# Optimization experiments

Measured on AMD Instinct MI355X. Metric: run time of the kernel, lower is better.

Reference implementation:

```python
import jax, jax.numpy as jnp
import numpy as np

FEAT = 2048
NUM_CLASSES = 751
EPS = 1e-5


def setup_inputs() -> dict:
    key = jax.random.key(0)
    k1, k2, k3 = jax.random.split(key, 3)
    probe_x = jax.random.normal(k1, (64, FEAT), dtype=jnp.float32)
    gallery_x = jax.random.normal(k2, (256, FEAT), dtype=jnp.float32)
    # BatchNorm1d affine params (PyTorch init: gamma=1, beta=0)
    bn_gamma = jnp.ones((FEAT,), dtype=jnp.float32)
    bn_beta = jnp.zeros((FEAT,), dtype=jnp.float32)
    # classifier: weight ~ N(0, 0.001), bias = 0
    W = jax.random.normal(k3, (NUM_CLASSES, FEAT), dtype=jnp.float32) * 0.001
    b = jnp.zeros((NUM_CLASSES,), dtype=jnp.float32)
    return {"probe_x": probe_x, "gallery_x": gallery_x,
            "bn_gamma": bn_gamma, "bn_beta": bn_beta, "W": W, "b": b}


def reference(probe_x, gallery_x, bn_gamma, bn_beta, W, b):
    n_probe, feat = probe_x.shape
    n_gallery = gallery_x.shape[0]
    # broadcast squared difference: [Np, Ng, F]
    diff = jnp.square(probe_x[:, None, :] - gallery_x[None, :, :])
    d = diff.reshape(n_probe * n_gallery, feat)
    # BatchNorm1d in training mode: biased batch statistics over the batch dim
    mean = jnp.mean(d, axis=0)
    var = jnp.mean(jnp.square(d - mean), axis=0)
    bn = (d - mean) * (bn_gamma / jnp.sqrt(var + EPS)) + bn_beta
    # Linear classifier
    cls = jnp.einsum('nf,cf->nc', bn, W) + b
    return cls.reshape(n_probe, n_gallery, -1)
```

## Files before the change

kernel.cpp:

```cpp
#include <hip/hip_runtime.h>
#include <hip/hip_bf16.h>
#include <hip/hip_fp16.h>

#define FEAT 2048
#define NCLS 751
#define NPAD 768
#define NPRB 64
#define NGAL 256
#define WSCALE 256.0f

typedef _Float16 f16x8 __attribute__((ext_vector_type(8)));
typedef float f32x4 __attribute__((ext_vector_type(4)));

__device__ __forceinline__ unsigned short f2h_u(float x) {
  union { _Float16 h; unsigned short u; } v;
  v.h = (_Float16)x;
  return v.u;
}

__global__ void stats_kernel(const float* __restrict__ P, const float* __restrict__ G,
                             const float* __restrict__ gamma, const float* __restrict__ beta,
                             float* __restrict__ st) {
  int fx = threadIdx.x & 31, ry = threadIdx.x >> 5;
  int f = blockIdx.x * 32 + fx;
  float a1 = 0, a2 = 0, a3 = 0, a4 = 0;
  for (int r = ry; r < NPRB; r += 8) {
    float x = P[r * FEAT + f], x2 = x * x;
    a1 += x; a2 += x2; a3 += x2 * x; a4 += x2 * x2;
  }
  float b1 = 0, b2 = 0, b3 = 0, b4 = 0;
  for (int r = ry; r < NGAL; r += 8) {
    float x = G[r * FEAT + f], x2 = x * x;
    b1 += x; b2 += x2; b3 += x2 * x; b4 += x2 * x2;
  }
  __shared__ float red[8][8][32];
  float vals[8] = {a1, a2, a3, a4, b1, b2, b3, b4};
#pragma unroll
  for (int m = 0; m < 8; ++m) red[m][ry][fx] = vals[m];
  __syncthreads();
  if (ry == 0) {
    float mm[8];
#pragma unroll
    for (int m = 0; m < 8; ++m) {
      float sum = 0.f;
#pragma unroll
      for (int r = 0; r < 8; ++r) sum += red[m][r][fx];
      mm[m] = sum;
    }
    float M1p = mm[0] * (1.f / NPRB), M2p = mm[1] * (1.f / NPRB);
    float M3p = mm[2] * (1.f / NPRB), M4p = mm[3] * (1.f / NPRB);
    float M1g = mm[4] * (1.f / NGAL), M2g = mm[5] * (1.f / NGAL);
    float M3g = mm[6] * (1.f / NGAL), M4g = mm[7] * (1.f / NGAL);
    float mean = M2p - 2.f * M1p * M1g + M2g;
    float Ed2 = M4p - 4.f * M3p * M1g + 6.f * M2p * M2g - 4.f * M1p * M3g + M4g;
    float var = Ed2 - mean * mean;
    float sv = gamma[f] / sqrtf(var + 1e-5f);
    st[f] = sv;
    st[FEAT + f] = beta[f] - mean * sv;
  }
}

__global__ void prepb_kernel(const float* __restrict__ W, const float* __restrict__ st,
                             unsigned short* __restrict__ Wp) {
  int idx = (blockIdx.x * 256 + threadIdx.x) * 4;
  int c = idx >> 11, f = idx & (FEAT - 1);
  float4 w = make_float4(0.f, 0.f, 0.f, 0.f);
  if (c < NCLS) w = *(const float4*)(W + (size_t)c * FEAT + f);
  float4 sv = *(const float4*)(st + f);
  unsigned int u0 = (unsigned int)f2h_u(w.x * sv.x * WSCALE) |
                    ((unsigned int)f2h_u(w.y * sv.y * WSCALE) << 16);
  unsigned int u1 = (unsigned int)f2h_u(w.z * sv.z * WSCALE) |
                    ((unsigned int)f2h_u(w.w * sv.w * WSCALE) << 16);
  uint2 u; u.x = u0; u.y = u1;
  *(uint2*)(Wp + idx) = u;
}

__global__ void prepbias_kernel(const float* __restrict__ W, const float* __restrict__ b,
                                const float* __restrict__ st, float* __restrict__ bp) {
  int c = blockIdx.x;
  const float* t = st + FEAT;
  float acc = 0.f;
  for (int f = threadIdx.x; f < FEAT; f += 256) acc += t[f] * W[(size_t)c * FEAT + f];
#pragma unroll
  for (int off = 32; off > 0; off >>= 1) acc += __shfl_down(acc, off, 64);
  __shared__ float r[4];
  int wave = threadIdx.x >> 6, lane = threadIdx.x & 63;
  if (lane == 0) r[wave] = acc;
  __syncthreads();
  if (threadIdx.x == 0) bp[c] = b[c] + r[0] + r[1] + r[2] + r[3];
}

#define AS_STRIDE 56

__global__ __launch_bounds__(256, 3)
void gemm_kernel(const float* __restrict__ P, const float* __restrict__ G,
                 const unsigned short* __restrict__ Wp, const float* __restrict__ bp,
                 float* __restrict__ out) {
  __shared__ float Prow[FEAT];
  __shared__ unsigned short As[128 * AS_STRIDE];
  __shared__ unsigned short Bs[128 * 32];

  const int tid = threadIdx.x;
  const int lane = tid & 63, wave = tid >> 6;
  const int mtile = blockIdx.x, ntile = blockIdx.y;
  const int p = mtile >> 1;
  const int g0 = (mtile & 1) * 128;

  const float4* psrc = (const float4*)(P + (size_t)p * FEAT);
  ((float4*)Prow)[tid] = psrc[tid];
  ((float4*)Prow)[tid + 256] = psrc[tid + 256];

  f32x4 acc[4][4];
#pragma unroll
  for (int mi = 0; mi < 4; ++mi)
#pragma unroll
    for (int ni = 0; ni < 4; ++ni) acc[mi][ni] = (f32x4){0.f, 0.f, 0.f, 0.f};

  const int wm = (wave & 1) * 64, wn = (wave >> 1) * 64;

  const int arow = tid >> 3, ac4 = tid & 7;
  const float* gbase = G + (size_t)(g0 + arow) * FEAT + ac4 * 4;
  unsigned short* awr = As + arow * AS_STRIDE + ac4 * 4;

  const int brow = tid >> 2, bchk = tid & 3;
  const unsigned short* bgbase = Wp + (size_t)(ntile * 128 + brow) * FEAT + bchk * 8;
  char* blds0 = (char*)Bs + wave * 1024;

  for (int k0 = 0; k0 < FEAT; k0 += 32) {
    __syncthreads();
    __builtin_amdgcn_global_load_lds(
        (const __attribute__((address_space(1))) void*)(bgbase + k0),
        (__attribute__((address_space(3))) void*)(blds0), 16, 0, 0);
    __builtin_amdgcn_global_load_lds(
        (const __attribute__((address_space(1))) void*)(bgbase + 64 * FEAT + k0),
        (__attribute__((address_space(3))) void*)(blds0 + 4096), 16, 0, 0);
    float4 p4 = *(const float4*)(Prow + k0 + ac4 * 4);
#pragma unroll
    for (int j = 0; j < 4; ++j) {
      float4 g4 = *(const float4*)(gbase + (size_t)j * 32 * FEAT + k0);
      float dx = p4.x - g4.x, dy = p4.y - g4.y;
      float dz = p4.z - g4.z, dw = p4.w - g4.w;
      uint2 u;
      u.x = (unsigned int)f2h_u(dx * dx) | ((unsigned int)f2h_u(dy * dy) << 16);
      u.y = (unsigned int)f2h_u(dz * dz) | ((unsigned int)f2h_u(dw * dw) << 16);
      *(uint2*)(awr + j * 32 * AS_STRIDE) = u;
    }
    __syncthreads();
    f16x8 af[4], bf[4];
#pragma unroll
    for (int mi = 0; mi < 4; ++mi)
      af[mi] = *(const f16x8*)(As + (wm + mi * 16 + (lane & 15)) * AS_STRIDE + (lane >> 4) * 8);
#pragma unroll
    for (int ni = 0; ni < 4; ++ni)
      bf[ni] = *(const f16x8*)(Bs + (wn + ni * 16 + (lane & 15)) * 32 + (lane >> 4) * 8);
#pragma unroll
    for (int mi = 0; mi < 4; ++mi)
#pragma unroll
      for (int ni = 0; ni < 4; ++ni)
        acc[mi][ni] = __builtin_amdgcn_mfma_f32_16x16x32_f16(af[mi], bf[ni], acc[mi][ni], 0, 0, 0);
  }

  const int col0 = ntile * 128 + wn + (lane & 15);
  const int row0 = mtile * 128 + wm + ((lane >> 4) << 2);
#pragma unroll
  for (int ni = 0; ni < 4; ++ni) {
    int col = col0 + ni * 16;
    if (col >= NCLS) continue;
    float bv = bp[col];
#pragma unroll
    for (int mi = 0; mi < 4; ++mi) {
      int row = row0 + mi * 16;
#pragma unroll
      for (int r = 0; r < 4; ++r)
        out[(size_t)(row + r) * NCLS + col] = acc[mi][ni][r] * (1.0f / WSCALE) + bv;
    }
  }
}

extern "C" void kernel_launch(void* const* d_in, const int* in_sizes, int n_in,
                              void* d_out, int out_size, void* d_ws, size_t ws_size,
                              hipStream_t stream) {
  const float* P = (const float*)d_in[0];
  const float* G = (const float*)d_in[1];
  const float* gamma = (const float*)d_in[2];
  const float* beta = (const float*)d_in[3];
  const float* W = (const float*)d_in[4];
  const float* b = (const float*)d_in[5];
  float* out = (float*)d_out;

  float* st = (float*)d_ws;
  float* bp = st + 2 * FEAT;
  unsigned short* Wp = (unsigned short*)(bp + NPAD);

  hipLaunchKernelGGL(stats_kernel, dim3(64), dim3(256), 0, stream, P, G, gamma, beta, st);
  hipLaunchKernelGGL(prepb_kernel, dim3(NPAD * FEAT / 1024), dim3(256), 0, stream, W, st, Wp);
  hipLaunchKernelGGL(prepbias_kernel, dim3(NCLS), dim3(256), 0, stream, W, b, st, bp);
  hipLaunchKernelGGL(gemm_kernel, dim3(128, 6), dim3(256), 0, stream, P, G, Wp, bp, out);
}
```

Baseline: 184.4 us.

## Materialize fp16 squared-difference matrix then run plain GEMM

Adds a kernel that writes the full probe-gallery squared-difference matrix in fp16 to workspace. A simpler GEMM then streams both operands via direct global-to-LDS loads. This removes the per-tile on-the-fly conversion that was repeated for every class tile. In exchange it adds a large extra write and read of a 64 MB intermediate. The old fused kernel is kept as a fallback when the workspace is too small.

```diff
diff --git a/kernel.cpp b/kernel.cpp
--- a/kernel.cpp
+++ b/kernel.cpp
@@ -90,12 +90,103 @@
   if (threadIdx.x == 0) bp[c] = b[c] + r[0] + r[1] + r[2] + r[3];
 }
 
+__global__ void agen_kernel(const float* __restrict__ P, const float* __restrict__ G,
+                            unsigned short* __restrict__ A) {
+  int n = blockIdx.x;
+  int p = n >> 8, g = n & 255;
+  int f = threadIdx.x * 8;
+  const float4* p4 = (const float4*)(P + (size_t)p * FEAT + f);
+  const float4* g4 = (const float4*)(G + (size_t)g * FEAT + f);
+  float4 pa = p4[0], pb = p4[1];
+  float4 ga = g4[0], gb = g4[1];
+  float d0 = pa.x - ga.x, d1 = pa.y - ga.y, d2 = pa.z - ga.z, d3 = pa.w - ga.w;
+  float d4 = pb.x - gb.x, d5 = pb.y - gb.y, d6 = pb.z - gb.z, d7 = pb.w - gb.w;
+  uint4 u;
+  u.x = (unsigned int)f2h_u(d0 * d0) | ((unsigned int)f2h_u(d1 * d1) << 16);
+  u.y = (unsigned int)f2h_u(d2 * d2) | ((unsigned int)f2h_u(d3 * d3) << 16);
+  u.z = (unsigned int)f2h_u(d4 * d4) | ((unsigned int)f2h_u(d5 * d5) << 16);
+  u.w = (unsigned int)f2h_u(d6 * d6) | ((unsigned int)f2h_u(d7 * d7) << 16);
+  *(uint4*)(A + (size_t)n * FEAT + f) = u;
+}
+
+__global__ __launch_bounds__(256, 3)
+void gemm_mat_kernel(const unsigned short* __restrict__ A,
+                     const unsigned short* __restrict__ Wp,
+                     const float* __restrict__ bp, float* __restrict__ out) {
+  __shared__ unsigned short As[128 * 32];
+  __shared__ unsigned short Bs[128 * 32];
+
+  const int tid = threadIdx.x;
+  const int lane = tid & 63, wave = tid >> 6;
+  const int mtile = blockIdx.x, ntile = blockIdx.y;
+
+  const int srow = tid >> 2, schk = tid & 3;
+  const unsigned short* ag = A + (size_t)(mtile * 128 + srow) * FEAT + schk * 8;
+  const unsigned short* bg = Wp + (size_t)(ntile * 128 + srow) * FEAT + schk * 8;
+  char* alds = (char*)As + wave * 1024;
+  char* blds = (char*)Bs + wave * 1024;
+
+  f32x4 acc[4][4];
+#pragma unroll
+  for (int mi = 0; mi < 4; ++mi)
+#pragma unroll
+    for (int ni = 0; ni < 4; ++ni) acc[mi][ni] = (f32x4){0.f, 0.f, 0.f, 0.f};
+
+  const int wm = (wave & 1) * 64, wn = (wave >> 1) * 64;
+
+  for (int k0 = 0; k0 < FEAT; k0 += 32) {
+    __syncthreads();
+    __builtin_amdgcn_global_load_lds(
+        (const __attribute__((address_space(1))) void*)(ag + k0),
+        (__attribute__((address_space(3))) void*)(alds), 16, 0, 0);
+    __builtin_amdgcn_global_load_lds(
+        (const __attribute__((address_space(1))) void*)(ag + (size_t)64 * FEAT + k0),
+        (__attribute__((address_space(3))) void*)(alds + 4096), 16, 0, 0);
+    __builtin_amdgcn_global_load_lds(
+        (const __attribute__((address_space(1))) void*)(bg + k0),
+        (__attribute__((address_space(3))) void*)(blds), 16, 0, 0);
+    __builtin_amdgcn_global_load_lds(
+        (const __attribute__((address_space(1))) void*)(bg + (size_t)64 * FEAT + k0),
+        (__attribute__((address_space(3))) void*)(blds + 4096), 16, 0, 0);
+    __syncthreads();
+
+    f16x8 af[4], bf[4];
+#pragma unroll
+    for (int mi = 0; mi < 4; ++mi)
+      af[mi] = *(const f16x8*)(As + (wm + mi * 16 + (lane & 15)) * 32 + (lane >> 4) * 8);
+#pragma unroll
+    for (int ni = 0; ni < 4; ++ni)
+      bf[ni] = *(const f16x8*)(Bs + (wn + ni * 16 + (lane & 15)) * 32 + (lane >> 4) * 8);
+#pragma unroll
+    for (int mi = 0; mi < 4; ++mi)
+#pragma unroll
+      for (int ni = 0; ni < 4; ++ni)
+        acc[mi][ni] = __builtin_amdgcn_mfma_f32_16x16x32_f16(af[mi], bf[ni], acc[mi][ni], 0, 0, 0);
+  }
+
+  const int col0 = ntile * 128 + wn + (lane & 15);
+  const int row0 = mtile * 128 + wm + ((lane >> 4) << 2);
+#pragma unroll
+  for (int ni = 0; ni < 4; ++ni) {
+    int col = col0 + ni * 16;
+    if (col >= NCLS) continue;
+    float bv = bp[col];
+#pragma unroll
+    for (int mi = 0; mi < 4; ++mi) {
+      int row = row0 + mi * 16;
+#pragma unroll
+      for (int r = 0; r < 4; ++r)
+        out[(size_t)(row + r) * NCLS + col] = acc[mi][ni][r] * (1.0f / WSCALE) + bv;
+    }
+  }
+}
+
 #define AS_STRIDE 56
 
 __global__ __launch_bounds__(256, 3)
-void gemm_kernel(const float* __restrict__ P, const float* __restrict__ G,
-                 const unsigned short* __restrict__ Wp, const float* __restrict__ bp,
-                 float* __restrict__ out) {
+void gemm_fly_kernel(const float* __restrict__ P, const float* __restrict__ G,
+                     const unsigned short* __restrict__ Wp, const float* __restrict__ bp,
+                     float* __restrict__ out) {
   __shared__ float Prow[FEAT];
   __shared__ unsigned short As[128 * AS_STRIDE];
   __shared__ unsigned short Bs[128 * 32];
@@ -117,11 +208,9 @@
     for (int ni = 0; ni < 4; ++ni) acc[mi][ni] = (f32x4){0.f, 0.f, 0.f, 0.f};
 
   const int wm = (wave & 1) * 64, wn = (wave >> 1) * 64;
-
   const int arow = tid >> 3, ac4 = tid & 7;
   const float* gbase = G + (size_t)(g0 + arow) * FEAT + ac4 * 4;
   unsigned short* awr = As + arow * AS_STRIDE + ac4 * 4;
-
   const int brow = tid >> 2, bchk = tid & 3;
   const unsigned short* bgbase = Wp + (size_t)(ntile * 128 + brow) * FEAT + bchk * 8;
   char* blds0 = (char*)Bs + wave * 1024;
@@ -191,9 +280,19 @@
   float* st = (float*)d_ws;
   float* bp = st + 2 * FEAT;
   unsigned short* Wp = (unsigned short*)(bp + NPAD);
+  unsigned short* A = Wp + (size_t)NPAD * FEAT;
+
+  size_t need = (size_t)(2 * FEAT + NPAD) * 4 + (size_t)NPAD * FEAT * 2 +
+                (size_t)NPRB * NGAL * FEAT * 2;
 
   hipLaunchKernelGGL(stats_kernel, dim3(64), dim3(256), 0, stream, P, G, gamma, beta, st);
   hipLaunchKernelGGL(prepb_kernel, dim3(NPAD * FEAT / 1024), dim3(256), 0, stream, W, st, Wp);
   hipLaunchKernelGGL(prepbias_kernel, dim3(NCLS), dim3(256), 0, stream, W, b, st, bp);
-  hipLaunchKernelGGL(gemm_kernel, dim3(128, 6), dim3(256), 0, stream, P, G, Wp, bp, out);
-}
+
+  if (ws_size >= need) {
+    hipLaunchKernelGGL(agen_kernel, dim3(NPRB * NGAL), dim3(256), 0, stream, P, G, A);
+    hipLaunchKernelGGL(gemm_mat_kernel, dim3(128, 6), dim3(256), 0, stream, A, Wp, bp, out);
+  } else {
+    hipLaunchKernelGGL(gemm_fly_kernel, dim3(128, 6), dim3(256), 0, stream, P, G, Wp, bp, out);
+  }
+}
```

Result: faster. 179.6 us (-2.6%).

## Materialize fp16 squared-difference matrix and stream both GEMM operands via LDS DMA

Applied to the files above, without the earlier changes.

Adds a separate kernel that writes the full 16384x2048 fp16 squared-difference matrix to workspace, so the GEMM loads both A and B with global_load_lds and an XOR-swizzled LDS layout instead of computing A inline from P and G. The K step grows from 32 to 64, which halves the barrier count. The W prep and bias kernels are merged into one kernel. The cost is writing and re-reading about 64 MB of A, read once per N tile, in exchange for removing per-tile VALU conversion and global float loads from the GEMM's critical path.

```diff
diff --git a/kernel.cpp b/kernel.cpp
--- a/kernel.cpp
+++ b/kernel.cpp
@@ -60,55 +60,73 @@
   }
 }
 
-__global__ void prepb_kernel(const float* __restrict__ W, const float* __restrict__ st,
-                             unsigned short* __restrict__ Wp) {
-  int idx = (blockIdx.x * 256 + threadIdx.x) * 4;
-  int c = idx >> 11, f = idx & (FEAT - 1);
-  float4 w = make_float4(0.f, 0.f, 0.f, 0.f);
-  if (c < NCLS) w = *(const float4*)(W + (size_t)c * FEAT + f);
-  float4 sv = *(const float4*)(st + f);
-  unsigned int u0 = (unsigned int)f2h_u(w.x * sv.x * WSCALE) |
-                    ((unsigned int)f2h_u(w.y * sv.y * WSCALE) << 16);
-  unsigned int u1 = (unsigned int)f2h_u(w.z * sv.z * WSCALE) |
-                    ((unsigned int)f2h_u(w.w * sv.w * WSCALE) << 16);
-  uint2 u; u.x = u0; u.y = u1;
-  *(uint2*)(Wp + idx) = u;
-}
-
-__global__ void prepbias_kernel(const float* __restrict__ W, const float* __restrict__ b,
-                                const float* __restrict__ st, float* __restrict__ bp) {
+__global__ void prepw_kernel(const float* __restrict__ W, const float* __restrict__ b,
+                             const float* __restrict__ st,
+                             unsigned short* __restrict__ Wp, float* __restrict__ bp) {
   int c = blockIdx.x;
-  const float* t = st + FEAT;
-  float acc = 0.f;
-  for (int f = threadIdx.x; f < FEAT; f += 256) acc += t[f] * W[(size_t)c * FEAT + f];
+  int f = threadIdx.x * 8;
+  float4 w0 = make_float4(0.f, 0.f, 0.f, 0.f), w1 = w0;
+  if (c < NCLS) {
+    const float4* wsrc = (const float4*)(W + (size_t)c * FEAT + f);
+    w0 = wsrc[0]; w1 = wsrc[1];
+  }
+  const float4* s4 = (const float4*)(st + f);
+  float4 s0 = s4[0], s1 = s4[1];
+  const float4* t4 = (const float4*)(st + FEAT + f);
+  float4 t0 = t4[0], t1 = t4[1];
+  uint4 u;
+  u.x = (unsigned int)f2h_u(w0.x * s0.x * WSCALE) | ((unsigned int)f2h_u(w0.y * s0.y * WSCALE) << 16);
+  u.y = (unsigned int)f2h_u(w0.z * s0.z * WSCALE) | ((unsigned int)f2h_u(w0.w * s0.w * WSCALE) << 16);
+  u.z = (unsigned int)f2h_u(w1.x * s1.x * WSCALE) | ((unsigned int)f2h_u(w1.y * s1.y * WSCALE) << 16);
+  u.w = (unsigned int)f2h_u(w1.z * s1.z * WSCALE) | ((unsigned int)f2h_u(w1.w * s1.w * WSCALE) << 16);
+  *(uint4*)(Wp + (size_t)c * FEAT + f) = u;
+  float acc = t0.x * w0.x + t0.y * w0.y + t0.z * w0.z + t0.w * w0.w +
+              t1.x * w1.x + t1.y * w1.y + t1.z * w1.z + t1.w * w1.w;
 #pragma unroll
   for (int off = 32; off > 0; off >>= 1) acc += __shfl_down(acc, off, 64);
   __shared__ float r[4];
   int wave = threadIdx.x >> 6, lane = threadIdx.x & 63;
   if (lane == 0) r[wave] = acc;
   __syncthreads();
-  if (threadIdx.x == 0) bp[c] = b[c] + r[0] + r[1] + r[2] + r[3];
-}
-
-#define AS_STRIDE 56
+  if (threadIdx.x == 0) bp[c] = (c < NCLS ? b[c] : 0.f) + r[0] + r[1] + r[2] + r[3];
+}
+
+__global__ void agen_kernel(const float* __restrict__ P, const float* __restrict__ G,
+                            unsigned short* __restrict__ A) {
+  int n = blockIdx.x;
+  int p = n >> 8, g = n & 255;
+  int f = threadIdx.x * 8;
+  const float4* p4 = (const float4*)(P + (size_t)p * FEAT + f);
+  const float4* g4 = (const float4*)(G + (size_t)g * FEAT + f);
+  float4 pa = p4[0], pb = p4[1];
+  float4 ga = g4[0], gb = g4[1];
+  float d0 = pa.x - ga.x, d1 = pa.y - ga.y, d2 = pa.z - ga.z, d3 = pa.w - ga.w;
+  float d4 = pb.x - gb.x, d5 = pb.y - gb.y, d6 = pb.z - gb.z, d7 = pb.w - gb.w;
+  uint4 u;
+  u.x = (unsigned int)f2h_u(d0 * d0) | ((unsigned int)f2h_u(d1 * d1) << 16);
+  u.y = (unsigned int)f2h_u(d2 * d2) | ((unsigned int)f2h_u(d3 * d3) << 16);
+  u.z = (unsigned int)f2h_u(d4 * d4) | ((unsigned int)f2h_u(d5 * d5) << 16);
+  u.w = (unsigned int)f2h_u(d6 * d6) | ((unsigned int)f2h_u(d7 * d7) << 16);
+  *(uint4*)(A + (size_t)n * FEAT + f) = u;
+}
 
 __global__ __launch_bounds__(256, 3)
-void gemm_kernel(const float* __restrict__ P, const float* __restrict__ G,
-                 const unsigned short* __restrict__ Wp, const float* __restrict__ bp,
-                 float* __restrict__ out) {
-  __shared__ float Prow[FEAT];
-  __shared__ unsigned short As[128 * AS_STRIDE];
-  __shared__ unsigned short Bs[128 * 32];
+void gemm_mat_kernel(const unsigned short* __restrict__ A,
+                     const unsigned short* __restrict__ Wp,
+                     const float* __restrict__ bp, float* __restrict__ out) {
+  __shared__ unsigned short As[128 * 64];
+  __shared__ unsigned short Bs[128 * 64];
 
   const int tid = threadIdx.x;
   const int lane = tid & 63, wave = tid >> 6;
   const int mtile = blockIdx.x, ntile = blockIdx.y;
-  const int p = mtile >> 1;
-  const int g0 = (mtile & 1) * 128;
-
-  const float4* psrc = (const float4*)(P + (size_t)p * FEAT);
-  ((float4*)Prow)[tid] = psrc[tid];
-  ((float4*)Prow)[tid + 256] = psrc[tid + 256];
+
+  const int srow = tid >> 3;
+  const int sch = (tid & 7) ^ (srow & 7);
+  const unsigned short* ag = A + (size_t)(mtile * 128 + srow) * FEAT + sch * 8;
+  const unsigned short* bg = Wp + (size_t)(ntile * 128 + srow) * FEAT + sch * 8;
+  char* alds = (char*)As + wave * 1024;
+  char* blds = (char*)Bs + wave * 1024;
 
   f32x4 acc[4][4];
 #pragma unroll
@@ -117,47 +135,37 @@
     for (int ni = 0; ni < 4; ++ni) acc[mi][ni] = (f32x4){0.f, 0.f, 0.f, 0.f};
 
   const int wm = (wave & 1) * 64, wn = (wave >> 1) * 64;
-
-  const int arow = tid >> 3, ac4 = tid & 7;
-  const float* gbase = G + (size_t)(g0 + arow) * FEAT + ac4 * 4;
-  unsigned short* awr = As + arow * AS_STRIDE + ac4 * 4;
-
-  const int brow = tid >> 2, bchk = tid & 3;
-  const unsigned short* bgbase = Wp + (size_t)(ntile * 128 + brow) * FEAT + bchk * 8;
-  char* blds0 = (char*)Bs + wave * 1024;
-
-  for (int k0 = 0; k0 < FEAT; k0 += 32) {
+  const int frow = lane & 15, fsw = lane & 7, fk = lane >> 4;
+
+  for (int k0 = 0; k0 < FEAT; k0 += 64) {
     __syncthreads();
-    __builtin_amdgcn_global_load_lds(
-        (const __attribute__((address_space(1))) void*)(bgbase + k0),
-        (__attribute__((address_space(3))) void*)(blds0), 16, 0, 0);
-    __builtin_amdgcn_global_load_lds(
-        (const __attribute__((address_space(1))) void*)(bgbase + 64 * FEAT + k0),
-        (__attribute__((address_space(3))) void*)(blds0 + 4096), 16, 0, 0);
-    float4 p4 = *(const float4*)(Prow + k0 + ac4 * 4);
 #pragma unroll
     for (int j = 0; j < 4; ++j) {
-      float4 g4 = *(const float4*)(gbase + (size_t)j * 32 * FEAT + k0);
-      float dx = p4.x - g4.x, dy = p4.y - g4.y;
-      float dz = p4.z - g4.z, dw = p4.w - g4.w;
-      uint2 u;
-      u.x = (unsigned int)f2h_u(dx * dx) | ((unsigned int)f2h_u(dy * dy) << 16);
-      u.y = (unsigned int)f2h_u(dz * dz) | ((unsigned int)f2h_u(dw * dw) << 16);
-      *(uint2*)(awr + j * 32 * AS_STRIDE) = u;
+      __builtin_amdgcn_global_load_lds(
+          (const __attribute__((address_space(1))) void*)(ag + k0 + (size_t)j * 32 * FEAT),
+          (__attribute__((address_space(3))) void*)(alds + j * 4096), 16, 0, 0);
+      __builtin_amdgcn_global_load_lds(
+          (const __attribute__((address_space(1))) void*)(bg + k0 + (size_t)j * 32 * FEAT),
+          (__attribute__((address_space(3))) void*)(blds + j * 4096), 16, 0, 0);
     }
     __syncthreads();
-    f16x8 af[4], bf[4];
-#pragma unroll
-    for (int mi = 0; mi < 4; ++mi)
-      af[mi] = *(const f16x8*)(As + (wm + mi * 16 + (lane & 15)) * AS_STRIDE + (lane >> 4) * 8);
-#pragma unroll
-    for (int ni = 0; ni < 4; ++ni)
-      bf[ni] = *(const f16x8*)(Bs + (wn + ni * 16 + (lane & 15)) * 32 + (lane >> 4) * 8);
-#pragma unroll
-    for (int mi = 0; mi < 4; ++mi)
+
+#pragma unroll
+    for (int kk = 0; kk < 2; ++kk) {
+      const int slot = (kk * 4 + fk) ^ fsw;
+      f16x8 af[4], bf[4];
+#pragma unroll
+      for (int mi = 0; mi < 4; ++mi)
+        af[mi] = *(const f16x8*)(As + (wm + mi * 16 + frow) * 64 + slot * 8);
 #pragma unroll
       for (int ni = 0; ni < 4; ++ni)
-        acc[mi][ni] = __builtin_amdgcn_mfma_f32_16x16x32_f16(af[mi], bf[ni], acc[mi][ni], 0, 0, 0);
+        bf[ni] = *(const f16x8*)(Bs + (wn + ni * 16 + frow) * 64 + slot * 8);
+#pragma unroll
+      for (int mi = 0; mi < 4; ++mi)
+#pragma unroll
+        for (int ni = 0; ni < 4; ++ni)
+          acc[mi][ni] = __builtin_amdgcn_mfma_f32_16x16x32_f16(af[mi], bf[ni], acc[mi][ni], 0, 0, 0);
+    }
   }
 
   const int col0 = ntile * 128 + wn + (lane & 15);
@@ -191,9 +199,10 @@
   float* st = (float*)d_ws;
   float* bp = st + 2 * FEAT;
   unsigned short* Wp = (unsigned short*)(bp + NPAD);
-
+  unsigned short* A = Wp + (size_t)NPAD * FEAT;
+
+  hipLaunchKernelGGL(agen_kernel, dim3(NPRB * NGAL), dim3(256), 0, stream, P, G, A);
   hipLaunchKernelGGL(stats_kernel, dim3(64), dim3(256), 0, stream, P, G, gamma, beta, st);
-  hipLaunchKernelGGL(prepb_kernel, dim3(NPAD * FEAT / 1024), dim3(256), 0, stream, W, st, Wp);
-  hipLaunchKernelGGL(prepbias_kernel, dim3(NCLS), dim3(256), 0, stream, W, b, st, bp);
-  hipLaunchKernelGGL(gemm_kernel, dim3(128, 6), dim3(256), 0, stream, P, G, Wp, bp, out);
-}
+  hipLaunchKernelGGL(prepw_kernel, dim3(NPAD), dim3(256), 0, stream, W, b, st, Wp, bp);
+  hipLaunchKernelGGL(gemm_mat_kernel, dim3(128, 6), dim3(256), 0, stream, A, Wp, bp, out);
+}
```

Result: faster. 166.8 us (-9.5%).
